# Optimization experiments

Hardware: AMD Instinct MI355X
Metric: run time of the kernel (lower is better)

Reference implementation:

```python
import jax, jax.numpy as jnp
import numpy as np

B, T, D = 2, 2048, 1024
H = 16
HD = D // H

def setup_inputs() -> dict:
    key = jax.random.key(0)
    ks = jax.random.split(key, 5)
    s = 1.0 / np.sqrt(D)
    return {
        "x": jax.random.normal(ks[0], (B, T, D), dtype=jnp.float32),
        "Wq": jax.random.normal(ks[1], (D, D), dtype=jnp.float32) * s,
        "bq": jnp.zeros((D,), jnp.float32),
        "Wk": jax.random.normal(ks[2], (D, D), dtype=jnp.float32) * s,
        "bk": jnp.zeros((D,), jnp.float32),
        "Wv": jax.random.normal(ks[3], (D, D), dtype=jnp.float32) * s,
        "bv": jnp.zeros((D,), jnp.float32),
        "Wo": jax.random.normal(ks[4], (D, D), dtype=jnp.float32) * s,
        "bo": jnp.zeros((D,), jnp.float32),
    }

def reference(x, Wq, bq, Wk, bk, Wv, bv, Wo, bo):
    # projections: torch Linear computes x @ W.T + b
    def split_heads(t):  # [B,T,D] -> [B,H,T,HD]
        return t.reshape(B, T, H, HD).transpose(0, 2, 1, 3)
    q = split_heads(x @ Wq.T + bq)
    k = split_heads(x @ Wk.T + bk)
    v = split_heads(x @ Wv.T + bv)
    scale = 1.0 / jnp.sqrt(jnp.asarray(HD, x.dtype))
    scores = jnp.einsum("bhtd,bhsd->bhts", q, k) * scale  # [B,H,T,T]
    causal = jnp.tril(jnp.ones((T, T), bool))
    scores = jnp.where(causal, scores, -jnp.inf)
    attn = jax.nn.softmax(scores, axis=-1)
    out = jnp.einsum("bhts,bhsd->bhtd", attn, v)  # [B,H,T,HD]
    out = out.transpose(0, 2, 1, 3).reshape(B, T, D)
    return out @ Wo.T + bo
```

## Files before the change

### kernel.cpp

```cpp
#include <hip/hip_runtime.h>
#include <hip/hip_bf16.h>

#define B_NUM 2
#define T_LEN 2048
#define D_DIM 1024
#define H_NUM 16
#define HD_DIM 64

#define Q_PRESCALE 0.18033688011112042f

using bf16x8 = __attribute__((ext_vector_type(8))) short;
using f32x4  = __attribute__((ext_vector_type(4))) float;
using u16x4  = __attribute__((ext_vector_type(4))) unsigned short;

__device__ __forceinline__ unsigned short f2bf(float f) {
    union { __hip_bfloat16 b; unsigned short u; } v;
    v.b = __float2bfloat16(f);
    return v.u;
}

__device__ __forceinline__ unsigned pack2bf(float a, float b) {
    union { __hip_bfloat162 h; unsigned u; } v;
    v.h = __float22bfloat162_rn(float2{a, b});
    return v.u;
}

__device__ __forceinline__ void gload16(const unsigned short* g, unsigned short* l) {
    __builtin_amdgcn_global_load_lds(
        (const __attribute__((address_space(1))) void*)g,
        (__attribute__((address_space(3))) void*)l, 16, 0, 0);
}

__global__ __launch_bounds__(256) void cvt5(
    const float* __restrict__ s0, const float* __restrict__ s1, const float* __restrict__ s2,
    const float* __restrict__ s3, const float* __restrict__ s4,
    unsigned short* __restrict__ d0, unsigned short* __restrict__ d1, unsigned short* __restrict__ d2,
    unsigned short* __restrict__ d3, unsigned short* __restrict__ d4,
    int c0, int c1, int c2, int c3, int c4)
{
    const float* src; unsigned short* dst; int cnt;
    switch (blockIdx.z) {
        case 0: src = s0; dst = d0; cnt = c0; break;
        case 1: src = s1; dst = d1; cnt = c1; break;
        case 2: src = s2; dst = d2; cnt = c2; break;
        case 3: src = s3; dst = d3; cnt = c3; break;
        default: src = s4; dst = d4; cnt = c4; break;
    }
    const int stride = gridDim.x * 256 * 4;
    for (int i = (blockIdx.x * 256 + threadIdx.x) * 4; i < cnt; i += stride) {
        float4 v = *(const float4*)(src + i);
        u16x4 o = { f2bf(v.x), f2bf(v.y), f2bf(v.z), f2bf(v.w) };
        *(u16x4*)(dst + i) = o;
    }
}

__device__ __forceinline__ void tile128(
    const unsigned short* __restrict__ A, const unsigned short* __restrict__ Bm,
    int m0, int n0, int K, unsigned short* lds, f32x4 acc[4][4])
{
    const int tid  = threadIdx.x;
    const int lane = tid & 63, w = tid >> 6;
    const int g = lane >> 4, c = lane & 15;
    const int wr = w >> 1, wc = w & 1;
    const int srow = lane >> 2;
    const int sch  = lane & 3;
    const int scsw = sch ^ ((srow >> 1) & 3);
    const int chunk = w * 2;
    const int row0 = chunk * 16 + srow;
    const int row1 = row0 + 16;
    const int rsw = (c >> 1) & 3;

    #pragma unroll
    for (int mi = 0; mi < 4; ++mi)
        #pragma unroll
        for (int ni = 0; ni < 4; ++ni)
            acc[mi][ni] = (f32x4){0.f, 0.f, 0.f, 0.f};

    const unsigned short* gA0 = A  + (size_t)(m0 + row0) * K + scsw * 8;
    const unsigned short* gA1 = A  + (size_t)(m0 + row1) * K + scsw * 8;
    const unsigned short* gB0 = Bm + (size_t)(n0 + row0) * K + scsw * 8;
    const unsigned short* gB1 = Bm + (size_t)(n0 + row1) * K + scsw * 8;

    auto stage = [&](int buf, int k0) {
        unsigned short* bA = lds + buf * 8192;
        unsigned short* bB = bA + 4096;
        gload16(gA0 + k0, bA + chunk * 512);
        gload16(gA1 + k0, bA + (chunk + 1) * 512);
        gload16(gB0 + k0, bB + chunk * 512);
        gload16(gB1 + k0, bB + (chunk + 1) * 512);
    };

    auto kstep = [&](int buf) {
        __builtin_amdgcn_s_barrier();
        asm volatile("" ::: "memory");
        const unsigned short* bA = lds + buf * 8192;
        const unsigned short* bB = bA + 4096;
        bf16x8 af[4], bfr[4];
        #pragma unroll
        for (int mi = 0; mi < 4; ++mi)
            af[mi] = *(const bf16x8*)(bA + (wr * 64 + mi * 16 + c) * 32 + (g ^ rsw) * 8);
        #pragma unroll
        for (int ni = 0; ni < 4; ++ni)
            bfr[ni] = *(const bf16x8*)(bB + (wc * 64 + ni * 16 + c) * 32 + (g ^ rsw) * 8);
        #pragma unroll
        for (int mi = 0; mi < 4; ++mi)
            #pragma unroll
            for (int ni = 0; ni < 4; ++ni)
                acc[mi][ni] = __builtin_amdgcn_mfma_f32_16x16x32_bf16(af[mi], bfr[ni], acc[mi][ni], 0, 0, 0);
        asm volatile("s_waitcnt lgkmcnt(0)" ::: "memory");
        __builtin_amdgcn_s_barrier();
    };

    const int nsteps = K / 32;
    stage(0, 0);
    stage(1, 32);
    int buf = 0;
    #pragma unroll 1
    for (int t = 0; t + 2 < nsteps; ++t) {
        int nb = buf + 2; if (nb >= 3) nb -= 3;
        stage(nb, (t + 2) * 32);
        asm volatile("s_waitcnt vmcnt(8)" ::: "memory");
        kstep(buf);
        ++buf; if (buf == 3) buf = 0;
    }
    asm volatile("s_waitcnt vmcnt(4)" ::: "memory");
    kstep(buf);
    ++buf; if (buf == 3) buf = 0;
    asm volatile("s_waitcnt vmcnt(0)" ::: "memory");
    kstep(buf);
}

__global__ __launch_bounds__(256) void gemm_qkv(
    const unsigned short* __restrict__ X,
    const unsigned short* __restrict__ Wq, const unsigned short* __restrict__ Wk,
    const unsigned short* __restrict__ Wv,
    const float* __restrict__ bq, const float* __restrict__ bk, const float* __restrict__ bv,
    unsigned short* __restrict__ Oq, unsigned short* __restrict__ Ok, unsigned short* __restrict__ OvT)
{
    __shared__ __align__(16) unsigned short lds[3 * 8192];
    const int bsw = (blockIdx.x & 7) * 96 + (blockIdx.x >> 3);
    const int mt = bsw / 24;
    const int rr = bsw - mt * 24;
    const int z  = rr >> 3;
    const int nt = rr & 7;

    const int lane = threadIdx.x & 63, w = threadIdx.x >> 6;
    const int g = lane >> 4, c = lane & 15;
    const int wr = w >> 1, wc = w & 1;
    f32x4 acc[4][4];

    if (z < 2) {
        const unsigned short* W = z ? Wk : Wq;
        const float* bias       = z ? bk : bq;
        unsigned short* Ob      = z ? Ok : Oq;
        const float oscale      = z ? 1.0f : Q_PRESCALE;
        const int m0 = mt * 128, n0 = nt * 128;
        tile128(X, W, m0, n0, D_DIM, lds, acc);
        #pragma unroll
        for (int mi = 0; mi < 4; ++mi) {
            #pragma unroll
            for (int ni = 0; ni < 4; ++ni) {
                const int col = n0 + wc * 64 + ni * 16 + c;
                const int h = col >> 6, hd = col & 63;
                const float bb = bias[col];
                #pragma unroll
                for (int r = 0; r < 4; ++r) {
                    const int row = m0 + wr * 64 + mi * 16 + g * 4 + r;
                    const int b_ = row >> 11, t = row & (T_LEN - 1);
                    Ob[((size_t)((b_ * H_NUM + h) * T_LEN + t)) * HD_DIM + hd] =
                        f2bf((acc[mi][ni][r] + bb) * oscale);
                }
            }
        }
    } else {
        const int m0 = nt * 128, n0 = mt * 128;
        tile128(Wv, X, m0, n0, D_DIM, lds, acc);
        #pragma unroll
        for (int mi = 0; mi < 4; ++mi) {
            #pragma unroll
            for (int ni = 0; ni < 4; ++ni) {
                const int j = n0 + wc * 64 + ni * 16 + c;
                const int b_ = j >> 11, t = j & (T_LEN - 1);
                #pragma unroll
                for (int r = 0; r < 4; ++r) {
                    const int f = m0 + wr * 64 + mi * 16 + g * 4 + r;
                    OvT[(size_t)(b_ * D_DIM + f) * T_LEN + t] = f2bf(acc[mi][ni][r] + bv[f]);
                }
            }
        }
    }
}

__global__ __launch_bounds__(256) void gemm_out(
    const unsigned short* __restrict__ A, const unsigned short* __restrict__ W,
    const float* __restrict__ bias, float* __restrict__ Out)
{
    __shared__ __align__(16) unsigned short lds[3 * 8192];
    const int bsw = (blockIdx.x & 7) * 32 + (blockIdx.x >> 3);
    const int mt = bsw >> 3, nt = bsw & 7;
    const int lane = threadIdx.x & 63, w = threadIdx.x >> 6;
    const int g = lane >> 4, c = lane & 15;
    const int m0 = mt * 128, n0 = nt * 128;
    f32x4 acc[4][4];
    tile128(A, W, m0, n0, D_DIM, lds, acc);
    const int wr = w >> 1, wc = w & 1;
    #pragma unroll
    for (int mi = 0; mi < 4; ++mi) {
        #pragma unroll
        for (int ni = 0; ni < 4; ++ni) {
            const int col = n0 + wc * 64 + ni * 16 + c;
            const float bb = bias[col];
            #pragma unroll
            for (int r = 0; r < 4; ++r) {
                const int row = m0 + wr * 64 + mi * 16 + g * 4 + r;
                Out[(size_t)row * D_DIM + col] = acc[mi][ni][r] + bb;
            }
        }
    }
}

__global__ __launch_bounds__(256, 4) void attn(
    const unsigned short* __restrict__ Q, const unsigned short* __restrict__ K,
    const unsigned short* __restrict__ VT, unsigned short* __restrict__ O)
{
    __shared__ __align__(16) unsigned short kv_lds[2][2][64 * 64];
    __shared__ __align__(16) unsigned short plbuf[4][16 * 64];
    const int tid = threadIdx.x, lane = tid & 63, w = tid >> 6;
    const int g = lane >> 4, c = lane & 15;

    const int gid = blockIdx.x;
    const int bh = gid & 31;
    const int jt = (gid < 512) ? (31 - (gid >> 5)) : ((gid - 512) >> 5);
    const int q0b = jt * 64;
    const int qw0 = q0b + w * 16;

    const unsigned short* Qb = Q  + (size_t)bh * T_LEN * HD_DIM;
    const unsigned short* Kb = K  + (size_t)bh * T_LEN * HD_DIM;
    const unsigned short* Vb = VT + (size_t)bh * HD_DIM * T_LEN;
    unsigned short* pl = plbuf[w];

    bf16x8 qf[2];
    #pragma unroll
    for (int kk = 0; kk < 2; ++kk)
        qf[kk] = *(const bf16x8*)(Qb + (size_t)(qw0 + c) * HD_DIM + kk * 32 + g * 8);

    f32x4 acc[4];
    #pragma unroll
    for (int ni = 0; ni < 4; ++ni) acc[ni] = (f32x4){0.f, 0.f, 0.f, 0.f};
    float m2 = -1e30f, l2 = 0.f;

    auto stage = [&](int buf, int kv0) {
        unsigned short* kb = &kv_lds[buf][0][0];
        unsigned short* vb = &kv_lds[buf][1][0];
        #pragma unroll
        for (int rnd = 0; rnd < 2; ++rnd) {
            const int bch = rnd * 256 + w * 64;
            const int row = (bch >> 3) + (lane >> 3);
            const int sc16 = (lane & 7) ^ (row & 7);
            gload16(Kb + (size_t)(kv0 + row) * HD_DIM + sc16 * 8, kb + bch * 8);
            gload16(Vb + (size_t)row * T_LEN + kv0 + sc16 * 8,   vb + bch * 8);
        }
    };

    const int ntiles = jt + 1;
    stage(0, 0);
    if (ntiles > 1) stage(1, 64);
    int cur = 0;
    #pragma unroll 1
    for (int t = 0; t < ntiles; ++t) {
        const int kv0 = t << 6;
        if (t + 1 < ntiles)
            asm volatile("s_waitcnt vmcnt(4)" ::: "memory");
        else
            asm volatile("s_waitcnt vmcnt(0)" ::: "memory");
        __builtin_amdgcn_s_barrier();
        const unsigned short* kb = &kv_lds[cur][0][0];
        const unsigned short* vb = &kv_lds[cur][1][0];

        f32x4 sf[4];
        #pragma unroll
        for (int st = 0; st < 4; ++st) {
            const int rr = st * 16 + c;
            bf16x8 kf0 = *(const bf16x8*)(kb + rr * 64 + ((g       ^ (c & 7)) * 8));
            bf16x8 kf1 = *(const bf16x8*)(kb + rr * 64 + (((4 + g) ^ (c & 7)) * 8));
            f32x4 s = (f32x4){0.f, 0.f, 0.f, 0.f};
            s = __builtin_amdgcn_mfma_f32_16x16x32_bf16(kf0, qf[0], s, 0, 0, 0);
            s = __builtin_amdgcn_mfma_f32_16x16x32_bf16(kf1, qf[1], s, 0, 0, 0);
            sf[st] = s;
        }
        if (t == jt) {
            const int qg = qw0 + c;
            #pragma unroll
            for (int st = 0; st < 4; ++st)
                #pragma unroll
                for (int r = 0; r < 4; ++r) {
                    const int kvg = kv0 + st * 16 + g * 4 + r;
                    sf[st][r] = (kvg <= qg) ? sf[st][r] : -1e30f;
                }
        }
        float ma = fmaxf(fmaxf(sf[0][0], sf[0][1]), sf[0][2]);
        float mb = fmaxf(fmaxf(sf[0][3], sf[1][0]), sf[1][1]);
        float mc = fmaxf(fmaxf(sf[1][2], sf[1][3]), sf[2][0]);
        float md = fmaxf(fmaxf(sf[2][1], sf[2][2]), sf[2][3]);
        float me = fmaxf(fmaxf(sf[3][0], sf[3][1]), sf[3][2]);
        float mx = fmaxf(fmaxf(fmaxf(ma, mb), fmaxf(mc, md)), fmaxf(me, sf[3][3]));
        mx = fmaxf(mx, __shfl_xor(mx, 16));
        mx = fmaxf(mx, __shfl_xor(mx, 32));
        if (__any(mx > m2 + 8.f)) {
            const float mnew = fmaxf(m2, mx);
            const float alpha = __builtin_amdgcn_exp2f(m2 - mnew);
            float ar[4];
            #pragma unroll
            for (int r = 0; r < 4; ++r) ar[r] = __shfl(alpha, g * 4 + r);
            l2 *= alpha;
            #pragma unroll
            for (int ni = 0; ni < 4; ++ni)
                #pragma unroll
                for (int r = 0; r < 4; ++r) acc[ni][r] *= ar[r];
            m2 = mnew;
        }
        float sum = 0.f;
        #pragma unroll
        for (int st = 0; st < 4; ++st)
            #pragma unroll
            for (int r = 0; r < 4; ++r) {
                const float p = __builtin_amdgcn_exp2f(sf[st][r] - m2);
                sf[st][r] = p;
                sum += p;
            }
        sum += __shfl_xor(sum, 16);
        sum += __shfl_xor(sum, 32);
        l2 += sum;
        #pragma unroll
        for (int st = 0; st < 4; ++st) {
            uint2 pk;
            pk.x = pack2bf(sf[st][0], sf[st][1]);
            pk.y = pack2bf(sf[st][2], sf[st][3]);
            const int idx = (c * 64 + st * 16 + g * 4) ^ ((c & 7) << 3);
            *(uint2*)(pl + idx) = pk;
        }
        asm volatile("" ::: "memory");
        bf16x8 pa[2];
        #pragma unroll
        for (int kk = 0; kk < 2; ++kk) {
            const int ridx = (c * 64 + kk * 32 + g * 8) ^ ((c & 7) << 3);
            pa[kk] = *(const bf16x8*)(pl + ridx);
        }
        #pragma unroll
        for (int ni = 0; ni < 4; ++ni) {
            const int rr = ni * 16 + c;
            bf16x8 vf0 = *(const bf16x8*)(vb + rr * 64 + ((g       ^ (c & 7)) * 8));
            bf16x8 vf1 = *(const bf16x8*)(vb + rr * 64 + (((4 + g) ^ (c & 7)) * 8));
            acc[ni] = __builtin_amdgcn_mfma_f32_16x16x32_bf16(pa[0], vf0, acc[ni], 0, 0, 0);
            acc[ni] = __builtin_amdgcn_mfma_f32_16x16x32_bf16(pa[1], vf1, acc[ni], 0, 0, 0);
        }
        asm volatile("s_waitcnt lgkmcnt(0)" ::: "memory");
        __builtin_amdgcn_s_barrier();
        if (t + 2 < ntiles) stage(cur, (t + 2) << 6);
        cur ^= 1;
    }

    const float linv = 1.0f / l2;
    float lr[4];
    #pragma unroll
    for (int r = 0; r < 4; ++r) lr[r] = __shfl(linv, g * 4 + r);
    const int b_ = bh >> 4, h = bh & 15;
    #pragma unroll
    for (int ni = 0; ni < 4; ++ni)
        #pragma unroll
        for (int r = 0; r < 4; ++r) {
            const int q = qw0 + g * 4 + r;
            O[(size_t)(b_ * T_LEN + q) * D_DIM + h * HD_DIM + ni * 16 + c] =
                f2bf(acc[ni][r] * lr[r]);
        }
}

extern "C" void kernel_launch(void* const* d_in, const int* in_sizes, int n_in,
                              void* d_out, int out_size, void* d_ws, size_t ws_size,
                              hipStream_t stream)
{
    const float* x  = (const float*)d_in[0];
    const float* Wq = (const float*)d_in[1];
    const float* bq = (const float*)d_in[2];
    const float* Wk = (const float*)d_in[3];
    const float* bk = (const float*)d_in[4];
    const float* Wv = (const float*)d_in[5];
    const float* bv = (const float*)d_in[6];
    const float* Wo = (const float*)d_in[7];
    const float* bo = (const float*)d_in[8];
    float* out = (float*)d_out;

    char* ws = (char*)d_ws;
    const size_t MB = 1u << 20;
    unsigned short* xb  = (unsigned short*)(ws + 0 * MB);
    unsigned short* wqb = (unsigned short*)(ws + 8 * MB);
    unsigned short* wkb = (unsigned short*)(ws + 10 * MB);
    unsigned short* wvb = (unsigned short*)(ws + 12 * MB);
    unsigned short* wob = (unsigned short*)(ws + 14 * MB);
    unsigned short* qw  = (unsigned short*)(ws + 16 * MB);
    unsigned short* kw  = (unsigned short*)(ws + 24 * MB);
    unsigned short* vtw = (unsigned short*)(ws + 32 * MB);
    unsigned short* ow  = (unsigned short*)(ws + 40 * MB);

    cvt5<<<dim3(1024, 1, 5), dim3(256), 0, stream>>>(
        x, Wq, Wk, Wv, Wo, xb, wqb, wkb, wvb, wob,
        B_NUM * T_LEN * D_DIM, D_DIM * D_DIM, D_DIM * D_DIM, D_DIM * D_DIM, D_DIM * D_DIM);

    gemm_qkv<<<dim3(768), dim3(256), 0, stream>>>(
        xb, wqb, wkb, wvb, bq, bk, bv, qw, kw, vtw);

    attn<<<dim3(1024), dim3(256), 0, stream>>>(qw, kw, vtw, ow);

    gemm_out<<<dim3(256), dim3(256), 0, stream>>>(
        ow, wob, bo, out);
}
```

Before: 101.8 us.

## Load K fragments directly into registers instead of staging through LDS

K tiles no longer go through shared memory. Each wave loads its MFMA K fragments straight from global memory into registers one tile ahead, and only V stays double-buffered in LDS. This cuts LDS footprint and LDS read traffic for K, which may allow higher occupancy. In exchange each of the four waves loads the same K tile redundantly, global loads become uncoalesced 16-byte row reads, and the vmcnt accounting now mixes register loads with async LDS loads, so the wait counts must stay correct.

Measured after the change: 134.6 us. +32.3%, slower.

```diff
diff --git a/kernel.cpp b/kernel.cpp
--- a/kernel.cpp
+++ b/kernel.cpp
@@ -223,7 +223,7 @@
     const unsigned short* __restrict__ Q, const unsigned short* __restrict__ K,
     const unsigned short* __restrict__ VT, unsigned short* __restrict__ O)
 {
-    __shared__ __align__(16) unsigned short kv_lds[2][2][64 * 64];
+    __shared__ __align__(16) unsigned short kv_lds[2][64 * 64];
     __shared__ __align__(16) unsigned short plbuf[4][16 * 64];
     const int tid = threadIdx.x, lane = tid & 63, w = tid >> 6;
     const int g = lane >> 4, c = lane & 15;
@@ -249,45 +249,51 @@
     for (int ni = 0; ni < 4; ++ni) acc[ni] = (f32x4){0.f, 0.f, 0.f, 0.f};
     float m2 = -1e30f, l2 = 0.f;
 
-    auto stage = [&](int buf, int kv0) {
-        unsigned short* kb = &kv_lds[buf][0][0];
-        unsigned short* vb = &kv_lds[buf][1][0];
+    bf16x8 kfr[4][2];
+    auto loadK = [&](int kv0) {
+        #pragma unroll
+        for (int st = 0; st < 4; ++st)
+            #pragma unroll
+            for (int kk = 0; kk < 2; ++kk)
+                kfr[st][kk] = *(const bf16x8*)(Kb + (size_t)(kv0 + st * 16 + c) * HD_DIM + kk * 32 + g * 8);
+    };
+
+    auto stageV = [&](int buf, int kv0) {
+        unsigned short* vb = &kv_lds[buf][0];
         #pragma unroll
         for (int rnd = 0; rnd < 2; ++rnd) {
             const int bch = rnd * 256 + w * 64;
             const int row = (bch >> 3) + (lane >> 3);
             const int sc16 = (lane & 7) ^ (row & 7);
-            gload16(Kb + (size_t)(kv0 + row) * HD_DIM + sc16 * 8, kb + bch * 8);
-            gload16(Vb + (size_t)row * T_LEN + kv0 + sc16 * 8,   vb + bch * 8);
+            gload16(Vb + (size_t)row * T_LEN + kv0 + sc16 * 8, vb + bch * 8);
         }
     };
 
     const int ntiles = jt + 1;
-    stage(0, 0);
-    if (ntiles > 1) stage(1, 64);
+    stageV(0, 0);
+    loadK(0);
+    if (ntiles > 1) stageV(1, 64);
     int cur = 0;
     #pragma unroll 1
     for (int t = 0; t < ntiles; ++t) {
         const int kv0 = t << 6;
         if (t + 1 < ntiles)
-            asm volatile("s_waitcnt vmcnt(4)" ::: "memory");
+            asm volatile("s_waitcnt vmcnt(2)" ::: "memory");
         else
             asm volatile("s_waitcnt vmcnt(0)" ::: "memory");
         __builtin_amdgcn_s_barrier();
-        const unsigned short* kb = &kv_lds[cur][0][0];
-        const unsigned short* vb = &kv_lds[cur][1][0];
+        const unsigned short* vb = &kv_lds[cur][0];
 
         f32x4 sf[4];
         #pragma unroll
         for (int st = 0; st < 4; ++st) {
-            const int rr = st * 16 + c;
-            bf16x8 kf0 = *(const bf16x8*)(kb + rr * 64 + ((g       ^ (c & 7)) * 8));
-            bf16x8 kf1 = *(const bf16x8*)(kb + rr * 64 + (((4 + g) ^ (c & 7)) * 8));
             f32x4 s = (f32x4){0.f, 0.f, 0.f, 0.f};
-            s = __builtin_amdgcn_mfma_f32_16x16x32_bf16(kf0, qf[0], s, 0, 0, 0);
-            s = __builtin_amdgcn_mfma_f32_16x16x32_bf16(kf1, qf[1], s, 0, 0, 0);
+            s = __builtin_amdgcn_mfma_f32_16x16x32_bf16(kfr[st][0], qf[0], s, 0, 0, 0);
+            s = __builtin_amdgcn_mfma_f32_16x16x32_bf16(kfr[st][1], qf[1], s, 0, 0, 0);
             sf[st] = s;
         }
+        if (t + 1 < ntiles) loadK(kv0 + 64);
+
         if (t == jt) {
             const int qg = qw0 + c;
             #pragma unroll
@@ -356,7 +362,7 @@
         }
         asm volatile("s_waitcnt lgkmcnt(0)" ::: "memory");
         __builtin_amdgcn_s_barrier();
-        if (t + 2 < ntiles) stage(cur, (t + 2) << 6);
+        if (t + 2 < ntiles) stageV(cur, (t + 2) << 6);
         cur ^= 1;
     }
 
```

## Double attention query tile per block to 128 rows, two 16-row strips per wave

Applied to the files above, without the earlier changes.

Each attention block now handles 128 query rows instead of 64, and each wave processes two 16-row strips. Every K/V tile staged into LDS is therefore reused by twice as many MFMAs, which halves K/V global traffic and the number of barriers per query row. The grid shrinks to 512 blocks and the occupancy hint in launch bounds is dropped. In exchange, register pressure and LDS use go up, there are fewer blocks to balance the causal workload, and waves whose strip lies entirely above the diagonal sit idle for some tiles.

New measurement: 118.8 us. +16.7%, slower.

```diff
diff --git a/kernel.cpp b/kernel.cpp
--- a/kernel.cpp
+++ b/kernel.cpp
@@ -219,35 +219,42 @@
     }
 }
 
-__global__ __launch_bounds__(256, 4) void attn(
+__global__ __launch_bounds__(256) void attn(
     const unsigned short* __restrict__ Q, const unsigned short* __restrict__ K,
     const unsigned short* __restrict__ VT, unsigned short* __restrict__ O)
 {
     __shared__ __align__(16) unsigned short kv_lds[2][2][64 * 64];
-    __shared__ __align__(16) unsigned short plbuf[4][16 * 64];
+    __shared__ __align__(16) unsigned short plbuf[4][32 * 64];
     const int tid = threadIdx.x, lane = tid & 63, w = tid >> 6;
     const int g = lane >> 4, c = lane & 15;
 
     const int gid = blockIdx.x;
     const int bh = gid & 31;
-    const int jt = (gid < 512) ? (31 - (gid >> 5)) : ((gid - 512) >> 5);
-    const int q0b = jt * 64;
-    const int qw0 = q0b + w * 16;
+    const int idx = gid >> 5;
+    const int jt = (idx < 8) ? (15 - idx) : (idx - 8);
+    const int q0b = jt << 7;
+    const int qw0 = q0b + w * 32;
 
     const unsigned short* Qb = Q  + (size_t)bh * T_LEN * HD_DIM;
     const unsigned short* Kb = K  + (size_t)bh * T_LEN * HD_DIM;
     const unsigned short* Vb = VT + (size_t)bh * HD_DIM * T_LEN;
     unsigned short* pl = plbuf[w];
 
-    bf16x8 qf[2];
+    bf16x8 qf[2][2];
     #pragma unroll
-    for (int kk = 0; kk < 2; ++kk)
-        qf[kk] = *(const bf16x8*)(Qb + (size_t)(qw0 + c) * HD_DIM + kk * 32 + g * 8);
-
-    f32x4 acc[4];
+    for (int mi = 0; mi < 2; ++mi)
+        #pragma unroll
+        for (int kk = 0; kk < 2; ++kk)
+            qf[mi][kk] = *(const bf16x8*)(Qb + (size_t)(qw0 + mi * 16 + c) * HD_DIM + kk * 32 + g * 8);
+
+    f32x4 acc[2][4];
+    float m2[2], l2[2];
     #pragma unroll
-    for (int ni = 0; ni < 4; ++ni) acc[ni] = (f32x4){0.f, 0.f, 0.f, 0.f};
-    float m2 = -1e30f, l2 = 0.f;
+    for (int mi = 0; mi < 2; ++mi) {
+        #pragma unroll
+        for (int ni = 0; ni < 4; ++ni) acc[mi][ni] = (f32x4){0.f, 0.f, 0.f, 0.f};
+        m2[mi] = -1e30f; l2[mi] = 0.f;
+    }
 
     auto stage = [&](int buf, int kv0) {
         unsigned short* kb = &kv_lds[buf][0][0];
@@ -262,9 +269,9 @@
         }
     };
 
-    const int ntiles = jt + 1;
+    const int ntiles = 2 * jt + 2;
     stage(0, 0);
-    if (ntiles > 1) stage(1, 64);
+    stage(1, 64);
     int cur = 0;
     #pragma unroll 1
     for (int t = 0; t < ntiles; ++t) {
@@ -274,85 +281,110 @@
         else
             asm volatile("s_waitcnt vmcnt(0)" ::: "memory");
         __builtin_amdgcn_s_barrier();
-        const unsigned short* kb = &kv_lds[cur][0][0];
-        const unsigned short* vb = &kv_lds[cur][1][0];
-
-        f32x4 sf[4];
-        #pragma unroll
-        for (int st = 0; st < 4; ++st) {
-            const int rr = st * 16 + c;
-            bf16x8 kf0 = *(const bf16x8*)(kb + rr * 64 + ((g       ^ (c & 7)) * 8));
-            bf16x8 kf1 = *(const bf16x8*)(kb + rr * 64 + (((4 + g) ^ (c & 7)) * 8));
-            f32x4 s = (f32x4){0.f, 0.f, 0.f, 0.f};
-            s = __builtin_amdgcn_mfma_f32_16x16x32_bf16(kf0, qf[0], s, 0, 0, 0);
-            s = __builtin_amdgcn_mfma_f32_16x16x32_bf16(kf1, qf[1], s, 0, 0, 0);
-            sf[st] = s;
-        }
-        if (t == jt) {
-            const int qg = qw0 + c;
-            #pragma unroll
-            for (int st = 0; st < 4; ++st)
-                #pragma unroll
-                for (int r = 0; r < 4; ++r) {
-                    const int kvg = kv0 + st * 16 + g * 4 + r;
-                    sf[st][r] = (kvg <= qg) ? sf[st][r] : -1e30f;
-                }
-        }
-        float ma = fmaxf(fmaxf(sf[0][0], sf[0][1]), sf[0][2]);
-        float mb = fmaxf(fmaxf(sf[0][3], sf[1][0]), sf[1][1]);
-        float mc = fmaxf(fmaxf(sf[1][2], sf[1][3]), sf[2][0]);
-        float md = fmaxf(fmaxf(sf[2][1], sf[2][2]), sf[2][3]);
-        float me = fmaxf(fmaxf(sf[3][0], sf[3][1]), sf[3][2]);
-        float mx = fmaxf(fmaxf(fmaxf(ma, mb), fmaxf(mc, md)), fmaxf(me, sf[3][3]));
-        mx = fmaxf(mx, __shfl_xor(mx, 16));
-        mx = fmaxf(mx, __shfl_xor(mx, 32));
-        if (__any(mx > m2 + 8.f)) {
-            const float mnew = fmaxf(m2, mx);
-            const float alpha = __builtin_amdgcn_exp2f(m2 - mnew);
-            float ar[4];
-            #pragma unroll
-            for (int r = 0; r < 4; ++r) ar[r] = __shfl(alpha, g * 4 + r);
-            l2 *= alpha;
-            #pragma unroll
-            for (int ni = 0; ni < 4; ++ni)
-                #pragma unroll
-                for (int r = 0; r < 4; ++r) acc[ni][r] *= ar[r];
-            m2 = mnew;
-        }
-        float sum = 0.f;
-        #pragma unroll
-        for (int st = 0; st < 4; ++st)
-            #pragma unroll
-            for (int r = 0; r < 4; ++r) {
-                const float p = __builtin_amdgcn_exp2f(sf[st][r] - m2);
-                sf[st][r] = p;
-                sum += p;
-            }
-        sum += __shfl_xor(sum, 16);
-        sum += __shfl_xor(sum, 32);
-        l2 += sum;
-        #pragma unroll
-        for (int st = 0; st < 4; ++st) {
-            uint2 pk;
-            pk.x = pack2bf(sf[st][0], sf[st][1]);
-            pk.y = pack2bf(sf[st][2], sf[st][3]);
-            const int idx = (c * 64 + st * 16 + g * 4) ^ ((c & 7) << 3);
-            *(uint2*)(pl + idx) = pk;
-        }
-        asm volatile("" ::: "memory");
-        bf16x8 pa[2];
-        #pragma unroll
-        for (int kk = 0; kk < 2; ++kk) {
-            const int ridx = (c * 64 + kk * 32 + g * 8) ^ ((c & 7) << 3);
-            pa[kk] = *(const bf16x8*)(pl + ridx);
-        }
-        #pragma unroll
-        for (int ni = 0; ni < 4; ++ni) {
-            const int rr = ni * 16 + c;
-            bf16x8 vf0 = *(const bf16x8*)(vb + rr * 64 + ((g       ^ (c & 7)) * 8));
-            bf16x8 vf1 = *(const bf16x8*)(vb + rr * 64 + (((4 + g) ^ (c & 7)) * 8));
-            acc[ni] = __builtin_amdgcn_mfma_f32_16x16x32_bf16(pa[0], vf0, acc[ni], 0, 0, 0);
-            acc[ni] = __builtin_amdgcn_mfma_f32_16x16x32_bf16(pa[1], vf1, acc[ni], 0, 0, 0);
+
+        if (kv0 <= qw0 + 31) {
+            const unsigned short* kb = &kv_lds[cur][0][0];
+            const unsigned short* vb = &kv_lds[cur][1][0];
+
+            f32x4 sf[2][4];
+            #pragma unroll
+            for (int st = 0; st < 4; ++st) {
+                const int rr = st * 16 + c;
+                bf16x8 kf0 = *(const bf16x8*)(kb + rr * 64 + ((g       ^ (c & 7)) * 8));
+                bf16x8 kf1 = *(const bf16x8*)(kb + rr * 64 + (((4 + g) ^ (c & 7)) * 8));
+                #pragma unroll
+                for (int mi = 0; mi < 2; ++mi) {
+                    f32x4 s = (f32x4){0.f, 0.f, 0.f, 0.f};
+                    s = __builtin_amdgcn_mfma_f32_16x16x32_bf16(kf0, qf[mi][0], s, 0, 0, 0);
+                    s = __builtin_amdgcn_mfma_f32_16x16x32_bf16(kf1, qf[mi][1], s, 0, 0, 0);
+                    sf[mi][st] = s;
+                }
+            }
+            if (kv0 + 63 > qw0) {
+                #pragma unroll
+                for (int mi = 0; mi < 2; ++mi) {
+                    const int qg = qw0 + mi * 16 + c;
+                    #pragma unroll
+                    for (int st = 0; st < 4; ++st)
+                        #pragma unroll
+                        for (int r = 0; r < 4; ++r) {
+                            const int kvg = kv0 + st * 16 + g * 4 + r;
+                            sf[mi][st][r] = (kvg <= qg) ? sf[mi][st][r] : -1e30f;
+                        }
+                }
+            }
+            float mx[2];
+            #pragma unroll
+            for (int mi = 0; mi < 2; ++mi) {
+                float ma = fmaxf(fmaxf(sf[mi][0][0], sf[mi][0][1]), sf[mi][0][2]);
+                float mb = fmaxf(fmaxf(sf[mi][0][3], sf[mi][1][0]), sf[mi][1][1]);
+                float mc = fmaxf(fmaxf(sf[mi][1][2], sf[mi][1][3]), sf[mi][2][0]);
+                float md = fmaxf(fmaxf(sf[mi][2][1], sf[mi][2][2]), sf[mi][2][3]);
+                float me = fmaxf(fmaxf(sf[mi][3][0], sf[mi][3][1]), sf[mi][3][2]);
+                float m = fmaxf(fmaxf(fmaxf(ma, mb), fmaxf(mc, md)), fmaxf(me, sf[mi][3][3]));
+                m = fmaxf(m, __shfl_xor(m, 16));
+                m = fmaxf(m, __shfl_xor(m, 32));
+                mx[mi] = m;
+            }
+            if (__any(fmaxf(mx[0] - m2[0], mx[1] - m2[1]) > 8.f)) {
+                #pragma unroll
+                for (int mi = 0; mi < 2; ++mi) {
+                    const float mnew = fmaxf(m2[mi], mx[mi]);
+                    const float alpha = __builtin_amdgcn_exp2f(m2[mi] - mnew);
+                    float ar[4];
+                    #pragma unroll
+                    for (int r = 0; r < 4; ++r) ar[r] = __shfl(alpha, g * 4 + r);
+                    l2[mi] *= alpha;
+                    #pragma unroll
+                    for (int ni = 0; ni < 4; ++ni)
+                        #pragma unroll
+                        for (int r = 0; r < 4; ++r) acc[mi][ni][r] *= ar[r];
+                    m2[mi] = mnew;
+                }
+            }
+            #pragma unroll
+            for (int mi = 0; mi < 2; ++mi) {
+                float sum = 0.f;
+                #pragma unroll
+                for (int st = 0; st < 4; ++st)
+                    #pragma unroll
+                    for (int r = 0; r < 4; ++r) {
+                        const float p = __builtin_amdgcn_exp2f(sf[mi][st][r] - m2[mi]);
+                        sf[mi][st][r] = p;
+                        sum += p;
+                    }
+                sum += __shfl_xor(sum, 16);
+                sum += __shfl_xor(sum, 32);
+                l2[mi] += sum;
+                #pragma unroll
+                for (int st = 0; st < 4; ++st) {
+                    uint2 pk;
+                    pk.x = pack2bf(sf[mi][st][0], sf[mi][st][1]);
+                    pk.y = pack2bf(sf[mi][st][2], sf[mi][st][3]);
+                    const int idx2 = ((mi * 16 + c) * 64 + st * 16 + g * 4) ^ ((c & 7) << 3);
+                    *(uint2*)(pl + idx2) = pk;
+                }
+            }
+            asm volatile("" ::: "memory");
+            bf16x8 pa[2][2];
+            #pragma unroll
+            for (int mi = 0; mi < 2; ++mi)
+                #pragma unroll
+                for (int kk = 0; kk < 2; ++kk) {
+                    const int ridx = ((mi * 16 + c) * 64 + kk * 32 + g * 8) ^ ((c & 7) << 3);
+                    pa[mi][kk] = *(const bf16x8*)(pl + ridx);
+                }
+            #pragma unroll
+            for (int ni = 0; ni < 4; ++ni) {
+                const int rr = ni * 16 + c;
+                bf16x8 vf0 = *(const bf16x8*)(vb + rr * 64 + ((g       ^ (c & 7)) * 8));
+                bf16x8 vf1 = *(const bf16x8*)(vb + rr * 64 + (((4 + g) ^ (c & 7)) * 8));
+                #pragma unroll
+                for (int mi = 0; mi < 2; ++mi) {
+                    acc[mi][ni] = __builtin_amdgcn_mfma_f32_16x16x32_bf16(pa[mi][0], vf0, acc[mi][ni], 0, 0, 0);
+                    acc[mi][ni] = __builtin_amdgcn_mfma_f32_16x16x32_bf16(pa[mi][1], vf1, acc[mi][ni], 0, 0, 0);
+                }
+            }
         }
         asm volatile("s_waitcnt lgkmcnt(0)" ::: "memory");
         __builtin_amdgcn_s_barrier();
@@ -360,19 +392,22 @@
         cur ^= 1;
     }
 
-    const float linv = 1.0f / l2;
-    float lr[4];
-    #pragma unroll
-    for (int r = 0; r < 4; ++r) lr[r] = __shfl(linv, g * 4 + r);
     const int b_ = bh >> 4, h = bh & 15;
     #pragma unroll
-    for (int ni = 0; ni < 4; ++ni)
-        #pragma unroll
-        for (int r = 0; r < 4; ++r) {
-            const int q = qw0 + g * 4 + r;
-            O[(size_t)(b_ * T_LEN + q) * D_DIM + h * HD_DIM + ni * 16 + c] =
-                f2bf(acc[ni][r] * lr[r]);
-        }
+    for (int mi = 0; mi < 2; ++mi) {
+        const float linv = 1.0f / l2[mi];
+        float lr[4];
+        #pragma unroll
+        for (int r = 0; r < 4; ++r) lr[r] = __shfl(linv, g * 4 + r);
+        #pragma unroll
+        for (int ni = 0; ni < 4; ++ni)
+            #pragma unroll
+            for (int r = 0; r < 4; ++r) {
+                const int q = qw0 + mi * 16 + g * 4 + r;
+                O[(size_t)(b_ * T_LEN + q) * D_DIM + h * HD_DIM + ni * 16 + c] =
+                    f2bf(acc[mi][ni][r] * lr[r]);
+            }
+    }
 }
 
 extern "C" void kernel_launch(void* const* d_in, const int* in_sizes, int n_in,
@@ -409,7 +444,7 @@
     gemm_qkv<<<dim3(768), dim3(256), 0, stream>>>(
         xb, wqb, wkb, wvb, bq, bk, bv, qw, kw, vtw);
 
-    attn<<<dim3(1024), dim3(256), 0, stream>>>(qw, kw, vtw, ow);
+    attn<<<dim3(512), dim3(256), 0, stream>>>(qw, kw, vtw, ow);
 
     gemm_out<<<dim3(256), dim3(256), 0, stream>>>(
         ow, wob, bo, out);
```
